# Kernel optimization log

Hardware: AMD Instinct MI355X
Metric: run time of the kernel (lower is better)

Reference implementation:

```python
import jax, jax.numpy as jnp
import numpy as np

DT = 0.1
EPS = 0.01


def _trans_layer(x, W, b):
    # x: [B, 2U]; W: [U, U]; b: [U]
    U = b.shape[0]
    t = DT / EPS
    u_in, v_in = x[:, :U], x[:, U:]
    act = jnp.tanh(u_in)
    v_star = (v_in + t * act) / (1.0 + t)
    # Block matrix A = [[I, dt*W], [-dt*W^T, I]] -- identical for all samples,
    # so factor/solve ONCE with a multi-RHS solve instead of torch's per-sample batched LU.
    I = jnp.eye(U, dtype=x.dtype)
    A = jnp.block([[I, DT * W], [-DT * W.T, I]])  # [2U, 2U]
    rhs = jnp.concatenate([u_in + DT * b, v_star], axis=1)  # [B, 2U]
    y = jnp.linalg.solve(A, rhs.T).T  # [B, 2U]
    u, v = y[:, :U], y[:, U:]
    u_out = DT * (v @ W.T) - u_in - DT * b
    v_out = -DT * (u @ W) + t * v - v_in - t * act
    return jnp.concatenate([u_out, v_out], axis=1)


def setup_inputs() -> dict:
    key = jax.random.key(0)
    ks = jax.random.split(key, 14)
    B, D_IN, U, D_OUT = 32768, 256, 256, 10

    def lin_w(k, o, i):
        return (jax.random.uniform(k, (o, i), jnp.float32) * 2.0 - 1.0) / np.sqrt(i).astype(np.float32)

    def lin_b(k, o, fan_in):
        return (jax.random.uniform(k, (o,), jnp.float32) * 2.0 - 1.0) / np.sqrt(fan_in).astype(np.float32)

    return {
        'x': jax.random.normal(ks[0], (B, D_IN), jnp.float32),
        'Wi': lin_w(ks[1], U, D_IN), 'bi': lin_b(ks[2], U, D_IN),
        'W1': lin_w(ks[3], U, U), 'b1': lin_b(ks[4], U, U),
        'W2': lin_w(ks[5], U, U), 'b2': lin_b(ks[6], U, U),
        'W3': lin_w(ks[7], U, U), 'b3': lin_b(ks[8], U, U),
        'W4': lin_w(ks[9], U, U), 'b4': lin_b(ks[10], U, U),
        'Wo': lin_w(ks[11], D_OUT, U), 'bo': lin_b(ks[12], D_OUT, U),
    }


def reference(x, Wi, bi, W1, b1, W2, b2, W3, b3, W4, b4, Wo, bo):
    U = W1.shape[0]
    z = x @ Wi.T + bi                       # linearInput
    z = jnp.concatenate([z, jnp.tanh(z)], axis=1)  # [B, 2U]
    for W, b in ((W1, b1), (W2, b2), (W3, b3), (W4, b4)):
        z = _trans_layer(z, W, b)
    z = z[:, :U]
    logits = z @ Wo.T + bo                  # linearOutput
    return jax.nn.softmax(logits, axis=1)
```

## Files before the change

kernel.cpp:

```cpp
#include <hip/hip_runtime.h>
#include <math.h>

#define DTC 0.1f

typedef _Float16 half8 __attribute__((ext_vector_type(8)));
typedef _Float16 half4v __attribute__((ext_vector_type(4)));
typedef float f32x4 __attribute__((ext_vector_type(4)));
typedef float f32x2 __attribute__((ext_vector_type(2)));

__device__ __forceinline__ float fast_tanh(float x) {
  const float e = __expf(2.f * x);
  const float r = __builtin_amdgcn_rcpf(e + 1.f);
  return fmaf(-2.f, r, 1.f);
}


__global__ __launch_bounds__(256) void k_prep(
    const float* __restrict__ W0, const float* __restrict__ W1,
    const float* __restrict__ W2, const float* __restrict__ W3,
    const float* __restrict__ b2, const float* __restrict__ b3,
    const float* __restrict__ b4,
    _Float16* __restrict__ Wh, _Float16* __restrict__ Wt,
    float* __restrict__ crm) {
  const float* Ws[4] = {W0, W1, W2, W3};
  const int bid = blockIdx.x, tid = threadIdx.x;
  if (bid < 128) {
    const int t = bid * 256 + tid;
    const float* W = Ws[(t * 8) >> 16];
    const int off = (t * 8) & 65535;
    const float4 a = *(const float4*)&W[off];
    const float4 b = *(const float4*)&W[off + 4];
    half8 h;
    h[0] = (_Float16)a.x; h[1] = (_Float16)a.y; h[2] = (_Float16)a.z; h[3] = (_Float16)a.w;
    h[4] = (_Float16)b.x; h[5] = (_Float16)b.y; h[6] = (_Float16)b.z; h[7] = (_Float16)b.w;
    *(half8*)&Wh[t * 8] = h;
  } else if (bid < 384) {
    __shared__ float sh[32][33];
    const int b2i = bid - 128;
    const int l = b2i >> 6, t64 = b2i & 63;
    const int r0 = (t64 >> 3) * 32, c0 = (t64 & 7) * 32;
    const float* W = Ws[l];
    const int i = tid >> 5, j = tid & 31;
#pragma unroll
    for (int p = 0; p < 4; ++p)
      sh[p * 8 + i][j] = W[(r0 + p * 8 + i) * 256 + c0 + j];
    __syncthreads();
#pragma unroll
    for (int p = 0; p < 4; ++p)
      Wt[l * 65536 + (c0 + p * 8 + i) * 256 + r0 + j] = (_Float16)sh[j][p * 8 + i];
  } else {
    const int l = bid - 384;
    const float* W = Ws[l];
    const float* b = (l == 0) ? b2 : (l == 1) ? b3 : b4;
    float s = 0.f;
#pragma unroll 8
    for (int k = 0; k < 256; ++k) s = fmaf(b[k], W[k * 256 + tid], s);
    crm[l * 256 + tid] = -0.09f * s;
  }
}

__global__ __launch_bounds__(256) void k_smm3(const _Float16* __restrict__ A,
                                              const _Float16* __restrict__ B,
                                              const _Float16* __restrict__ Eadd,
                                              _Float16* __restrict__ C,
                                              float scale, int addI) {
  const int tid = threadIdx.x, wave = tid >> 6, lane = tid & 63;
  const int quad = lane >> 4, l16 = lane & 15;
  const int l = blockIdx.z;
  const _Float16* Al = A + (size_t)l * 65536;
  const _Float16* Bl = B + (size_t)l * 65536;
  _Float16* Cl = C + (size_t)l * 65536;
  const int m0 = blockIdx.y * 64 + wave * 16, n0 = blockIdx.x * 64;
  f32x4 acc[4] = {};
#pragma unroll
  for (int kt = 0; kt < 8; ++kt) {
    const half8 af = *(const half8*)&Al[(m0 + l16) * 256 + kt * 32 + quad * 8];
#pragma unroll
    for (int ni = 0; ni < 4; ++ni) {
      const half8 bf = *(const half8*)&Bl[(n0 + ni * 16 + l16) * 256 + kt * 32 + quad * 8];
      acc[ni] = __builtin_amdgcn_mfma_f32_16x16x32_f16(af, bf, acc[ni], 0, 0, 0);
    }
  }
#pragma unroll
  for (int ni = 0; ni < 4; ++ni)
#pragma unroll
    for (int r = 0; r < 4; ++r) {
      const int row = m0 + quad * 4 + r, col = n0 + ni * 16 + l16;
      float v = scale * acc[ni][r];
      if (addI) v += (row == col ? 1.f : 0.f) - (float)(Eadd + (size_t)l * 65536)[row * 256 + col];
      Cl[row * 256 + col] = (_Float16)v;
    }
}

__global__ __launch_bounds__(256) void k_pack(
    const _Float16* __restrict__ Ph, const _Float16* __restrict__ Qt,
    const _Float16* __restrict__ Wt, const float* __restrict__ Wi,
    const float* __restrict__ Wo,
    _Float16* __restrict__ PQP, _Float16* __restrict__ RmP,
    _Float16* __restrict__ WiP, _Float16* __restrict__ WoP) {
  const int t = blockIdx.x * 256 + threadIdx.x;
  if (t < 65536) {
    const int l = t >> 14, c = t & 16383;
    const int ntile = c >> 10, kt = (c >> 6) & 15, lb = c & 63;
    const int n = ntile * 16 + (lb & 15);
    const int kq = (lb >> 4) * 8;
    half8 h;
    if (kt < 8) {
      h = *(const half8*)&Ph[(size_t)l * 65536 + n * 256 + kt * 32 + kq];
#pragma unroll
      for (int j = 0; j < 8; ++j) h[j] = -h[j];
    } else {
      h = *(const half8*)&Qt[(size_t)l * 65536 + n * 256 + (kt - 8) * 32 + kq];
    }
    *(half8*)&PQP[(size_t)t * 8] = h;
  } else if (t < 90112) {
    const int tt = t - 65536;
    const int l = tt >> 13, c = tt & 8191;
    const int ntile = c >> 9, kt = (c >> 6) & 7, lb = c & 63;
    const int n = ntile * 16 + (lb & 15);
    const int k0 = kt * 32 + (lb >> 4) * 8;
    half8 h = *(const half8*)&Wt[(size_t)l * 65536 + n * 256 + k0];
#pragma unroll
    for (int j = 0; j < 8; ++j) h[j] = (_Float16)(-0.9f * (float)h[j]);
    *(half8*)&RmP[(size_t)tt * 8] = h;
  } else if (t < 98304) {
    const int c = t - 90112;
    const int ntile = c >> 9, kt = (c >> 6) & 7, lb = c & 63;
    const int n = ntile * 16 + (lb & 15);
    const int k0 = kt * 32 + (lb >> 4) * 8;
    const float4 a = *(const float4*)&Wi[n * 256 + k0];
    const float4 b = *(const float4*)&Wi[n * 256 + k0 + 4];
    half8 h;
    h[0] = (_Float16)a.x; h[1] = (_Float16)a.y; h[2] = (_Float16)a.z; h[3] = (_Float16)a.w;
    h[4] = (_Float16)b.x; h[5] = (_Float16)b.y; h[6] = (_Float16)b.z; h[7] = (_Float16)b.w;
    *(half8*)&WiP[(size_t)c * 8] = h;
  } else {
    const int c = t - 98304;
    const int kt = c >> 6, lb = c & 63;
    const int n = lb & 15;
    const int k0 = kt * 32 + (lb >> 4) * 8;
    half8 h;
#pragma unroll
    for (int j = 0; j < 8; ++j) h[j] = (_Float16)((n < 10) ? Wo[n * 256 + k0 + j] : 0.f);
    *(half8*)&WoP[(size_t)c * 8] = h;
  }
}


__device__ __forceinline__ int lds_off4(int row, int col0) {
  const int chunk = (col0 >> 3) ^ (row & 7);
  return row * 512 + (chunk << 4) + (col0 & 7) * 2;
}

template <int NKT, bool DUAL>
__device__ __forceinline__ void gemm_k(const _Float16* __restrict__ Bp,
                                       const _Float16* A1, const _Float16* A2,
                                       f32x4* acc, int wave, int lane, int quad, int l16) {
  half8 bf[3][2];
  auto loadB = [&](int kt, int s) {
#pragma unroll
    for (int ni = 0; ni < 2; ++ni)
      bf[s][ni] = *(const half8*)&Bp[(((wave * 2 + ni) * NKT + kt) * 64 + lane) * 8];
  };
  loadB(0, 0);
  loadB(1, 1);
#pragma unroll
  for (int kt = 0; kt < NKT; ++kt) {
    const int s = kt % 3;
    if (kt + 2 < NKT) loadB(kt + 2, (kt + 2) % 3);
    const _Float16* Ab = (DUAL && kt >= NKT / 2) ? A2 : A1;
    const int akt = DUAL ? (kt & (NKT / 2 - 1)) : kt;
    half8 af[4];
#pragma unroll
    for (int mi = 0; mi < 4; ++mi) {
      const int row = mi * 16 + l16;
      const int chunk = (akt * 4 + quad) ^ (row & 7);
      af[mi] = *(const half8*)((const char*)Ab + row * 512 + (chunk << 4));
    }
#pragma unroll
    for (int mi = 0; mi < 4; ++mi)
#pragma unroll
      for (int ni = 0; ni < 2; ++ni)
        acc[mi * 2 + ni] = __builtin_amdgcn_mfma_f32_16x16x32_f16(
            bf[s][ni], af[mi], acc[mi * 2 + ni], 0, 0, 0);
  }
}

__global__ __launch_bounds__(512, 2) void k_fused(
    const float* __restrict__ x, const _Float16* __restrict__ WiP,
    const _Float16* __restrict__ PQP, const _Float16* __restrict__ RmP,
    const _Float16* __restrict__ WoP, const float* __restrict__ bi,
    const float* __restrict__ b1, const float* __restrict__ b2,
    const float* __restrict__ b3, const float* __restrict__ b4,
    const float* __restrict__ crm, const float* __restrict__ bo,
    float* __restrict__ out) {
  __shared__ __align__(16) _Float16 A1[64 * 256];
  __shared__ __align__(16) _Float16 A2[64 * 256];
  const int tid = threadIdx.x;
  const int wave = tid >> 6, lane = tid & 63;
  const int quad = lane >> 4, l16 = lane & 15;
  const int m0 = blockIdx.x * 64;

#pragma unroll
  for (int it = 0; it < 8; ++it) {
    const int idx = it * 512 + tid;
    const int row = idx >> 6, c4 = idx & 63;
    const float4 v = *(const float4*)&x[(size_t)(m0 + row) * 256 + c4 * 4];
    const int chunk = (c4 >> 1) ^ (row & 7), part = c4 & 1;
    _Float16* p = (_Float16*)((char*)A1 + row * 512 + (chunk << 4) + (part << 3));
    p[0] = (_Float16)v.x; p[1] = (_Float16)v.y; p[2] = (_Float16)v.z; p[3] = (_Float16)v.w;
  }
  __syncthreads();

  f32x4 acc[8];
  const f32x4 zero = {0.f, 0.f, 0.f, 0.f};
  half4v uph[8], r2p[8];

#pragma unroll
  for (int t = 0; t < 8; ++t) acc[t] = zero;
  gemm_k<8, false>(WiP, A1, A1, acc, wave, lane, quad, l16);
  __syncthreads();
#pragma unroll
  for (int ni = 0; ni < 2; ++ni) {
    const int col0 = wave * 32 + ni * 16 + quad * 4;
    const f32x4 bi4 = *(const f32x4*)&bi[col0];
    const f32x4 b14 = *(const f32x4*)&b1[col0];
#pragma unroll
    for (int mi = 0; mi < 4; ++mi) {
      const int row = mi * 16 + l16;
      const int off = lds_off4(row, col0);
      half4v h1, h2;
#pragma unroll
      for (int r = 0; r < 4; ++r) {
        const float z = acc[mi * 2 + ni][r] + bi4[r];
        h1[r] = (_Float16)(z + DTC * b14[r]);
        h2[r] = (_Float16)fast_tanh(z);
      }
      *(half4v*)((char*)A1 + off) = h1;
      *(half4v*)((char*)A2 + off) = h2;
      r2p[mi * 2 + ni] = h2;
    }
  }
  __syncthreads();

#pragma unroll 1
  for (int l = 0; l < 4; ++l) {
#pragma unroll
    for (int t = 0; t < 8; ++t) acc[t] = zero;
    gemm_k<16, true>(PQP + (size_t)l * 131072, A1, A2, acc, wave, lane, quad, l16);
    __syncthreads();
    const float* bn = (l == 0) ? b2 : (l == 1) ? b3 : b4;
#pragma unroll
    for (int ni = 0; ni < 2; ++ni) {
      const int col0 = wave * 32 + ni * 16 + quad * 4;
      f32x4 bn4 = zero;
      if (l < 3) bn4 = DTC * (*(const f32x4*)&bn[col0]);
#pragma unroll
      for (int mi = 0; mi < 4; ++mi) {
        const int row = mi * 16 + l16;
        const int off = lds_off4(row, col0);
        half4v hu, h1;
#pragma unroll
        for (int r = 0; r < 4; ++r) {
          const float u = acc[mi * 2 + ni][r];
          hu[r] = (_Float16)u;
          h1[r] = (_Float16)(u + bn4[r]);
        }
        uph[mi * 2 + ni] = hu;
        *(half4v*)((char*)A1 + off) = h1;
      }
    }
    __syncthreads();
    if (l < 3) {
#pragma unroll
      for (int t = 0; t < 8; ++t) acc[t] = zero;
      gemm_k<8, false>(RmP + (size_t)l * 65536, A1, A1, acc, wave, lane, quad, l16);
#pragma unroll
      for (int ni = 0; ni < 2; ++ni) {
        const int col0 = wave * 32 + ni * 16 + quad * 4;
        const f32x4 cc4 = *(const f32x4*)&crm[l * 256 + col0];
#pragma unroll
        for (int mi = 0; mi < 4; ++mi) {
          const int row = mi * 16 + l16;
          const int off = lds_off4(row, col0);
          half4v nr2;
#pragma unroll
          for (int r = 0; r < 4; ++r) {
            const float vp = acc[mi * 2 + ni][r] - cc4[r] - (float)r2p[mi * 2 + ni][r];
            nr2[r] = (_Float16)((vp + 10.f * fast_tanh((float)uph[mi * 2 + ni][r])) * (1.f / 11.f));
          }
          r2p[mi * 2 + ni] = nr2;
          *(half4v*)((char*)A2 + off) = nr2;
        }
      }
      __syncthreads();
    }
  }

  if (wave < 4) {
    f32x4 acch = zero;
#pragma unroll
    for (int kt = 0; kt < 8; ++kt) {
      const int row = wave * 16 + l16;
      const int chunk = (kt * 4 + quad) ^ (row & 7);
      const half8 af = *(const half8*)((const char*)A1 + row * 512 + (chunk << 4));
      const half8 bfr = *(const half8*)&WoP[(kt * 64 + lane) * 8];
      acch = __builtin_amdgcn_mfma_f32_16x16x32_f16(bfr, af, acch, 0, 0, 0);
    }
    float v4[4];
    float mx = -3.0e38f;
#pragma unroll
    for (int r = 0; r < 4; ++r) {
      const int cls = quad * 4 + r;
      const float v = acch[r] + ((cls < 10) ? bo[cls] : -3.0e38f);
      v4[r] = v;
      mx = fmaxf(mx, v);
    }
    mx = fmaxf(mx, __shfl_xor(mx, 16, 64));
    mx = fmaxf(mx, __shfl_xor(mx, 32, 64));
    float e4[4], s = 0.f;
#pragma unroll
    for (int r = 0; r < 4; ++r) {
      e4[r] = __expf(v4[r] - mx);
      s += e4[r];
    }
    s += __shfl_xor(s, 16, 64);
    s += __shfl_xor(s, 32, 64);
    const float rs = __builtin_amdgcn_rcpf(s);
    float* op = &out[(size_t)(m0 + wave * 16 + l16) * 10 + quad * 4];
    if (quad < 2) {
      f32x2 p0 = {e4[0] * rs, e4[1] * rs};
      f32x2 p1 = {e4[2] * rs, e4[3] * rs};
      *(f32x2*)op = p0;
      *(f32x2*)(op + 2) = p1;
    } else if (quad == 2) {
      f32x2 p0 = {e4[0] * rs, e4[1] * rs};
      *(f32x2*)op = p0;
    }
  }
}


extern "C" void kernel_launch(void* const* d_in, const int* in_sizes, int n_in,
                              void* d_out, int out_size, void* d_ws, size_t ws_size,
                              hipStream_t stream) {
  const float* x  = (const float*)d_in[0];
  const float* Wi = (const float*)d_in[1];
  const float* bi = (const float*)d_in[2];
  const float* W[4] = {(const float*)d_in[3], (const float*)d_in[5],
                       (const float*)d_in[7], (const float*)d_in[9]};
  const float* b[4] = {(const float*)d_in[4], (const float*)d_in[6],
                       (const float*)d_in[8], (const float*)d_in[10]};
  const float* Wo = (const float*)d_in[11];
  const float* bo = (const float*)d_in[12];
  float* out = (float*)d_out;

  const int Bsz = in_sizes[0] / 256;

  _Float16* hb = (_Float16*)d_ws;
  _Float16* WiP = hb;
  _Float16* WoP = hb + 65536;
  _Float16* PQP = hb + 69632;
  _Float16* RmP = hb + 593920;
  _Float16* Wh  = hb + 790528;
  _Float16* Wt  = hb + 1052672;
  _Float16* Eh  = hb + 1314816;
  _Float16* Ph  = hb + 1576960;
  _Float16* Qt  = hb + 1839104;
  float* crm = (float*)(hb + 2101248);

  const dim3 g64(4, 4, 4);
  k_prep<<<387, 256, 0, stream>>>(W[0], W[1], W[2], W[3], b[1], b[2], b[3],
                                  Wh, Wt, crm);
  k_smm3<<<g64, 256, 0, stream>>>(Wh, Wh, nullptr, Eh, 0.01f, 0);
  k_smm3<<<g64, 256, 0, stream>>>(Eh, Eh, Eh, Ph, 1.0f, 1);
  k_smm3<<<g64, 256, 0, stream>>>(Ph, Wt, nullptr, Qt, DTC, 0);
  k_pack<<<386, 256, 0, stream>>>(Ph, Qt, Wt, Wi, Wo, PQP, RmP, WiP, WoP);

  k_fused<<<Bsz / 64, 512, 0, stream>>>(x, WiP, PQP, RmP, WoP, bi,
                                        b[0], b[1], b[2], b[3], crm, bo, out);
}
```

Before: 204.0 us.

## Fold the per-layer v-update GEMM into the u GEMM via precomputed composite matrices

Precomputes composite matrices U = 0.9·Wᵀ·P and V = −0.1·U·Wᵀ per layer with extra small-matmul launches, and packs them as a second weight operand. The fused kernel then computes u and the v-update together in one dual-accumulator pass over the same LDS activations. This removes the separate dependent GEMM, its barriers and the LDS round trip of u in each of the first three layers. In exchange it issues more MFMA work per layer (K=512 for both outputs), doubles the accumulator registers under a tight 512-thread, 2-blocks-per-CU launch bound, and drops the crm bias correction term.

```diff
diff --git a/kernel.cpp b/kernel.cpp
--- a/kernel.cpp
+++ b/kernel.cpp
@@ -94,9 +94,9 @@
 
 __global__ __launch_bounds__(256) void k_pack(
     const _Float16* __restrict__ Ph, const _Float16* __restrict__ Qt,
-    const _Float16* __restrict__ Wt, const float* __restrict__ Wi,
-    const float* __restrict__ Wo,
-    _Float16* __restrict__ PQP, _Float16* __restrict__ RmP,
+    const _Float16* __restrict__ Uh, const _Float16* __restrict__ Vh,
+    const float* __restrict__ Wi, const float* __restrict__ Wo,
+    _Float16* __restrict__ PQP, _Float16* __restrict__ UVP,
     _Float16* __restrict__ WiP, _Float16* __restrict__ WoP) {
   const int t = blockIdx.x * 256 + threadIdx.x;
   if (t < 65536) {
@@ -113,18 +113,18 @@
       h = *(const half8*)&Qt[(size_t)l * 65536 + n * 256 + (kt - 8) * 32 + kq];
     }
     *(half8*)&PQP[(size_t)t * 8] = h;
-  } else if (t < 90112) {
+  } else if (t < 114688) {
     const int tt = t - 65536;
-    const int l = tt >> 13, c = tt & 8191;
-    const int ntile = c >> 9, kt = (c >> 6) & 7, lb = c & 63;
+    const int l = tt >> 14, c = tt & 16383;
+    const int ntile = c >> 10, kt = (c >> 6) & 15, lb = c & 63;
     const int n = ntile * 16 + (lb & 15);
-    const int k0 = kt * 32 + (lb >> 4) * 8;
-    half8 h = *(const half8*)&Wt[(size_t)l * 65536 + n * 256 + k0];
-#pragma unroll
-    for (int j = 0; j < 8; ++j) h[j] = (_Float16)(-0.9f * (float)h[j]);
-    *(half8*)&RmP[(size_t)tt * 8] = h;
-  } else if (t < 98304) {
-    const int c = t - 90112;
+    const int kq = (lb >> 4) * 8;
+    const _Float16* src = (kt < 8)
+        ? &Uh[(size_t)l * 65536 + n * 256 + kt * 32 + kq]
+        : &Vh[(size_t)l * 65536 + n * 256 + (kt - 8) * 32 + kq];
+    *(half8*)&UVP[(size_t)tt * 8] = *(const half8*)src;
+  } else if (t < 122880) {
+    const int c = t - 114688;
     const int ntile = c >> 9, kt = (c >> 6) & 7, lb = c & 63;
     const int n = ntile * 16 + (lb & 15);
     const int k0 = kt * 32 + (lb >> 4) * 8;
@@ -134,8 +134,8 @@
     h[0] = (_Float16)a.x; h[1] = (_Float16)a.y; h[2] = (_Float16)a.z; h[3] = (_Float16)a.w;
     h[4] = (_Float16)b.x; h[5] = (_Float16)b.y; h[6] = (_Float16)b.z; h[7] = (_Float16)b.w;
     *(half8*)&WiP[(size_t)c * 8] = h;
-  } else {
-    const int c = t - 98304;
+  } else if (t < 123392) {
+    const int c = t - 122880;
     const int kt = c >> 6, lb = c & 63;
     const int n = lb & 15;
     const int k0 = kt * 32 + (lb >> 4) * 8;
@@ -186,14 +186,53 @@
   }
 }
 
+__device__ __forceinline__ void gemm_uv(const _Float16* __restrict__ PQ,
+                                        const _Float16* __restrict__ UV,
+                                        const _Float16* A1, const _Float16* A2,
+                                        f32x4* accu, f32x4* accv,
+                                        int wave, int lane, int quad, int l16) {
+  half8 bfP[2][2], bfU[2][2];
+  auto loadB = [&](int kt, int s) {
+#pragma unroll
+    for (int ni = 0; ni < 2; ++ni) {
+      const int idx = (((wave * 2 + ni) * 16 + kt) * 64 + lane) * 8;
+      bfP[s][ni] = *(const half8*)&PQ[idx];
+      bfU[s][ni] = *(const half8*)&UV[idx];
+    }
+  };
+  loadB(0, 0);
+#pragma unroll
+  for (int kt = 0; kt < 16; ++kt) {
+    const int s = kt & 1;
+    if (kt + 1 < 16) loadB(kt + 1, (kt + 1) & 1);
+    const _Float16* Ab = (kt >= 8) ? A2 : A1;
+    const int akt = kt & 7;
+    half8 af[4];
+#pragma unroll
+    for (int mi = 0; mi < 4; ++mi) {
+      const int row = mi * 16 + l16;
+      const int chunk = (akt * 4 + quad) ^ (row & 7);
+      af[mi] = *(const half8*)((const char*)Ab + row * 512 + (chunk << 4));
+    }
+#pragma unroll
+    for (int mi = 0; mi < 4; ++mi)
+#pragma unroll
+      for (int ni = 0; ni < 2; ++ni) {
+        accu[mi * 2 + ni] = __builtin_amdgcn_mfma_f32_16x16x32_f16(
+            bfP[s][ni], af[mi], accu[mi * 2 + ni], 0, 0, 0);
+        accv[mi * 2 + ni] = __builtin_amdgcn_mfma_f32_16x16x32_f16(
+            bfU[s][ni], af[mi], accv[mi * 2 + ni], 0, 0, 0);
+      }
+  }
+}
+
 __global__ __launch_bounds__(512, 2) void k_fused(
     const float* __restrict__ x, const _Float16* __restrict__ WiP,
-    const _Float16* __restrict__ PQP, const _Float16* __restrict__ RmP,
+    const _Float16* __restrict__ PQP, const _Float16* __restrict__ UVP,
     const _Float16* __restrict__ WoP, const float* __restrict__ bi,
     const float* __restrict__ b1, const float* __restrict__ b2,
     const float* __restrict__ b3, const float* __restrict__ b4,
-    const float* __restrict__ crm, const float* __restrict__ bo,
-    float* __restrict__ out) {
+    const float* __restrict__ bo, float* __restrict__ out) {
   __shared__ __align__(16) _Float16 A1[64 * 256];
   __shared__ __align__(16) _Float16 A2[64 * 256];
   const int tid = threadIdx.x;
@@ -212,13 +251,13 @@
   }
   __syncthreads();
 
-  f32x4 acc[8];
+  f32x4 accu[8], accv[8];
   const f32x4 zero = {0.f, 0.f, 0.f, 0.f};
-  half4v uph[8], r2p[8];
-
-#pragma unroll
-  for (int t = 0; t < 8; ++t) acc[t] = zero;
-  gemm_k<8, false>(WiP, A1, A1, acc, wave, lane, quad, l16);
+  half4v r2p[8];
+
+#pragma unroll
+  for (int t = 0; t < 8; ++t) accu[t] = zero;
+  gemm_k<8, false>(WiP, A1, A1, accu, wave, lane, quad, l16);
   __syncthreads();
 #pragma unroll
   for (int ni = 0; ni < 2; ++ni) {
@@ -232,7 +271,7 @@
       half4v h1, h2;
 #pragma unroll
       for (int r = 0; r < 4; ++r) {
-        const float z = acc[mi * 2 + ni][r] + bi4[r];
+        const float z = accu[mi * 2 + ni][r] + bi4[r];
         h1[r] = (_Float16)(z + DTC * b14[r]);
         h2[r] = (_Float16)fast_tanh(z);
       }
@@ -244,58 +283,55 @@
   __syncthreads();
 
 #pragma unroll 1
-  for (int l = 0; l < 4; ++l) {
-#pragma unroll
-    for (int t = 0; t < 8; ++t) acc[t] = zero;
-    gemm_k<16, true>(PQP + (size_t)l * 131072, A1, A2, acc, wave, lane, quad, l16);
+  for (int l = 0; l < 3; ++l) {
+#pragma unroll
+    for (int t = 0; t < 8; ++t) { accu[t] = zero; accv[t] = zero; }
+    gemm_uv(PQP + (size_t)l * 131072, UVP + (size_t)l * 131072,
+            A1, A2, accu, accv, wave, lane, quad, l16);
     __syncthreads();
     const float* bn = (l == 0) ? b2 : (l == 1) ? b3 : b4;
 #pragma unroll
     for (int ni = 0; ni < 2; ++ni) {
       const int col0 = wave * 32 + ni * 16 + quad * 4;
-      f32x4 bn4 = zero;
-      if (l < 3) bn4 = DTC * (*(const f32x4*)&bn[col0]);
+      const f32x4 bn4 = DTC * (*(const f32x4*)&bn[col0]);
 #pragma unroll
       for (int mi = 0; mi < 4; ++mi) {
         const int row = mi * 16 + l16;
         const int off = lds_off4(row, col0);
-        half4v hu, h1;
+        half4v h1, nr2;
 #pragma unroll
         for (int r = 0; r < 4; ++r) {
-          const float u = acc[mi * 2 + ni][r];
-          hu[r] = (_Float16)u;
+          const float u = accu[mi * 2 + ni][r];
+          const float vp = accv[mi * 2 + ni][r] - (float)r2p[mi * 2 + ni][r];
+          nr2[r] = (_Float16)((vp + 10.f * fast_tanh(u)) * (1.f / 11.f));
           h1[r] = (_Float16)(u + bn4[r]);
         }
-        uph[mi * 2 + ni] = hu;
+        r2p[mi * 2 + ni] = nr2;
         *(half4v*)((char*)A1 + off) = h1;
+        *(half4v*)((char*)A2 + off) = nr2;
       }
     }
     __syncthreads();
-    if (l < 3) {
-#pragma unroll
-      for (int t = 0; t < 8; ++t) acc[t] = zero;
-      gemm_k<8, false>(RmP + (size_t)l * 65536, A1, A1, acc, wave, lane, quad, l16);
-#pragma unroll
-      for (int ni = 0; ni < 2; ++ni) {
-        const int col0 = wave * 32 + ni * 16 + quad * 4;
-        const f32x4 cc4 = *(const f32x4*)&crm[l * 256 + col0];
-#pragma unroll
-        for (int mi = 0; mi < 4; ++mi) {
-          const int row = mi * 16 + l16;
-          const int off = lds_off4(row, col0);
-          half4v nr2;
-#pragma unroll
-          for (int r = 0; r < 4; ++r) {
-            const float vp = acc[mi * 2 + ni][r] - cc4[r] - (float)r2p[mi * 2 + ni][r];
-            nr2[r] = (_Float16)((vp + 10.f * fast_tanh((float)uph[mi * 2 + ni][r])) * (1.f / 11.f));
-          }
-          r2p[mi * 2 + ni] = nr2;
-          *(half4v*)((char*)A2 + off) = nr2;
-        }
-      }
-      __syncthreads();
-    }
-  }
+  }
+
+#pragma unroll
+  for (int t = 0; t < 8; ++t) accu[t] = zero;
+  gemm_k<16, true>(PQP + (size_t)3 * 131072, A1, A2, accu, wave, lane, quad, l16);
+  __syncthreads();
+#pragma unroll
+  for (int ni = 0; ni < 2; ++ni) {
+    const int col0 = wave * 32 + ni * 16 + quad * 4;
+#pragma unroll
+    for (int mi = 0; mi < 4; ++mi) {
+      const int row = mi * 16 + l16;
+      const int off = lds_off4(row, col0);
+      half4v h1;
+#pragma unroll
+      for (int r = 0; r < 4; ++r) h1[r] = (_Float16)accu[mi * 2 + ni][r];
+      *(half4v*)((char*)A1 + off) = h1;
+    }
+  }
+  __syncthreads();
 
   if (wave < 4) {
     f32x4 acch = zero;
@@ -361,22 +397,27 @@
   _Float16* WiP = hb;
   _Float16* WoP = hb + 65536;
   _Float16* PQP = hb + 69632;
-  _Float16* RmP = hb + 593920;
-  _Float16* Wh  = hb + 790528;
-  _Float16* Wt  = hb + 1052672;
-  _Float16* Eh  = hb + 1314816;
-  _Float16* Ph  = hb + 1576960;
-  _Float16* Qt  = hb + 1839104;
-  float* crm = (float*)(hb + 2101248);
+  _Float16* UVP = hb + 593920;
+  _Float16* Wh  = hb + 987136;
+  _Float16* Wt  = hb + 1249280;
+  _Float16* Eh  = hb + 1511424;
+  _Float16* Ph  = hb + 1773568;
+  _Float16* Qt  = hb + 2035712;
+  _Float16* Uh  = hb + 2297856;
+  _Float16* Vh  = hb + 2494464;
+  float* crm = (float*)(hb + 2691072);
 
   const dim3 g64(4, 4, 4);
+  const dim3 g64_3(4, 4, 3);
   k_prep<<<387, 256, 0, stream>>>(W[0], W[1], W[2], W[3], b[1], b[2], b[3],
                                   Wh, Wt, crm);
   k_smm3<<<g64, 256, 0, stream>>>(Wh, Wh, nullptr, Eh, 0.01f, 0);
   k_smm3<<<g64, 256, 0, stream>>>(Eh, Eh, Eh, Ph, 1.0f, 1);
   k_smm3<<<g64, 256, 0, stream>>>(Ph, Wt, nullptr, Qt, DTC, 0);
-  k_pack<<<386, 256, 0, stream>>>(Ph, Qt, Wt, Wi, Wo, PQP, RmP, WiP, WoP);
-
-  k_fused<<<Bsz / 64, 512, 0, stream>>>(x, WiP, PQP, RmP, WoP, bi,
-                                        b[0], b[1], b[2], b[3], crm, bo, out);
-}
+  k_smm3<<<g64_3, 256, 0, stream>>>(Wt, Ph, nullptr, Uh, 0.9f, 0);
+  k_smm3<<<g64_3, 256, 0, stream>>>(Uh, Wt, nullptr, Vh, -0.1f, 0);
+  k_pack<<<482, 256, 0, stream>>>(Ph, Qt, Uh, Vh, Wi, Wo, PQP, UVP, WiP, WoP);
+
+  k_fused<<<Bsz / 64, 512, 0, stream>>>(x, WiP, PQP, UVP, WoP, bi,
+                                        b[0], b[1], b[2], b[3], bo, out);
+}
```

Result: slower. 234.7 us (+15.1%).
